# Kernel optimization log

Hardware: AMD Instinct MI355X
Metric: run time of the kernel (lower is better)

The kernel has to match this reference:

```python
import jax, jax.numpy as jnp
import numpy as np

B, N, D = 4, 2048, 1024
H, HD = 16, 64
MAX_SEQ = 4096
INNER = H * HD


def setup_inputs() -> dict:
    key = jax.random.key(0)
    ks = jax.random.split(key, 5)
    s = 0.02
    return {
        "x": jax.random.normal(ks[0], (B, N, D), dtype=jnp.float32),
        "ln_gamma": jnp.ones((D,), jnp.float32),
        "ln_beta": jnp.zeros((D,), jnp.float32),
        "w_qkv": jax.random.normal(ks[1], (D, 3 * INNER), dtype=jnp.float32) * s,
        "w_out": jax.random.normal(ks[2], (INNER, D), dtype=jnp.float32) * s,
        "b_out": jnp.zeros((D,), jnp.float32),
    }


def _rope_tables(n, head_dim):
    inv_freq = 1.0 / (10000.0 ** (jnp.arange(0, head_dim, 2, dtype=jnp.float32) / head_dim))
    pos = jnp.arange(n, dtype=jnp.float32)
    ang = pos[:, None] * inv_freq[None, :]  # [n, hd/2]
    return jnp.sin(ang), jnp.cos(ang)


def reference(x, ln_gamma, ln_beta, w_qkv, w_out, b_out):
    b, n, d = x.shape
    # LayerNorm
    mu = jnp.mean(x, axis=-1, keepdims=True)
    var = jnp.var(x, axis=-1, keepdims=True)
    xn = (x - mu) / jnp.sqrt(var + 1e-5) * ln_gamma + ln_beta
    # QKV projection (no bias)
    qkv = xn @ w_qkv  # [b, n, 3*inner]
    q, k, v = jnp.split(qkv, 3, axis=-1)
    def to_heads(t):
        return t.reshape(b, n, H, HD).transpose(0, 2, 1, 3)  # b h n d
    q, k, v = to_heads(q), to_heads(k), to_heads(v)
    # RoPE (half-split rotation, as in source)
    sin, cos = _rope_tables(n, HD)  # [n, hd/2]
    sin = sin[None, None]
    cos = cos[None, None]
    half = HD // 2
    def rotate(t):
        t1, t2 = t[..., :half], t[..., half:]
        return jnp.concatenate([t1 * cos - t2 * sin, t2 * cos + t1 * sin], axis=-1)
    qr, kr = rotate(q), rotate(k)
    scale = HD ** -0.5
    scores = jnp.einsum('bhid,bhjd->bhij', qr, kr) * scale
    probs = jax.nn.softmax(scores, axis=-1)
    out = jnp.einsum('bhij,bhjd->bhid', probs, v)
    out = out.transpose(0, 2, 1, 3).reshape(b, n, INNER)
    return out @ w_out + b_out
```

## Files before the change

kernel.cpp:

```cpp
#include <hip/hip_runtime.h>
#include <hip/hip_bf16.h>

#define Bb   4
#define Nn   2048
#define Dd   1024
#define Hh   16
#define HDd  64
#define IN3  3072
#define RR   8192

typedef __attribute__((ext_vector_type(8))) short short8;
typedef __attribute__((ext_vector_type(4))) short short4v;
typedef __attribute__((ext_vector_type(4))) float floatx4;

#define MFMA16(a, b, c) __builtin_amdgcn_mfma_f32_16x16x32_bf16((a), (b), (c), 0, 0, 0)

static __device__ __forceinline__ floatx4 mfma16x16x16(short4v a, short4v b, floatx4 c) {
#if __has_builtin(__builtin_amdgcn_mfma_f32_16x16x16bf16_1k)
    return __builtin_amdgcn_mfma_f32_16x16x16bf16_1k(a, b, c, 0, 0, 0);
#else
    floatx4 d;
    asm("v_mfma_f32_16x16x16_bf16 %0, %1, %2, %3" : "=v"(d) : "v"(a), "v"(b), "v"(c));
    return d;
#endif
}

static __device__ __forceinline__ unsigned short f2bf(float f) {
    union { float f; unsigned int u; } v; v.f = f;
    unsigned int r = v.u + 0x7fffu + ((v.u >> 16) & 1u);
    return (unsigned short)(r >> 16);
}
static __device__ __forceinline__ float bf2f(unsigned short h) {
    union { unsigned int u; float f; } v; v.u = ((unsigned int)h) << 16;
    return v.f;
}

static __device__ __forceinline__ float fast_exp2(float x) {
#if __has_builtin(__builtin_amdgcn_exp2f)
    return __builtin_amdgcn_exp2f(x);
#else
    return exp2f(x);
#endif
}

typedef const __attribute__((address_space(1))) void* gas1_t;
typedef __attribute__((address_space(3))) void* las3_t;
static __device__ __forceinline__ void load_lds16(const void* g, void* l) {
    __builtin_amdgcn_global_load_lds((gas1_t)(unsigned long long)g,
                                     (las3_t)(unsigned int)(unsigned long long)l,
                                     16, 0, 0);
}

__global__ void transpose_w(const float* __restrict__ src, unsigned short* __restrict__ dst,
                            int rows, int cols) {
    __shared__ float tile[32][33];
    int c0 = blockIdx.x * 32, r0 = blockIdx.y * 32;
    int tx = threadIdx.x, ty = threadIdx.y;
#pragma unroll
    for (int i = 0; i < 4; ++i) tile[ty + 8 * i][tx] = src[(r0 + ty + 8 * i) * cols + c0 + tx];
    __syncthreads();
#pragma unroll
    for (int i = 0; i < 4; ++i) dst[(c0 + ty + 8 * i) * rows + r0 + tx] = f2bf(tile[tx][ty + 8 * i]);
}

__global__ __launch_bounds__(256) void ln_kernel(const float* __restrict__ x,
                                                 const float* __restrict__ g,
                                                 const float* __restrict__ be,
                                                 unsigned short* __restrict__ xn) {
    int row = blockIdx.x, t = threadIdx.x;
    float4 v = ((const float4*)(x + row * Dd))[t];
    float s  = v.x + v.y + v.z + v.w;
    float sq = v.x * v.x + v.y * v.y + v.z * v.z + v.w * v.w;
#pragma unroll
    for (int off = 1; off < 64; off <<= 1) { s += __shfl_xor(s, off); sq += __shfl_xor(sq, off); }
    __shared__ float ps[4], pq2[4];
    int wv = t >> 6;
    if ((t & 63) == 0) { ps[wv] = s; pq2[wv] = sq; }
    __syncthreads();
    s  = ps[0] + ps[1] + ps[2] + ps[3];
    sq = pq2[0] + pq2[1] + pq2[2] + pq2[3];
    float mu   = s * (1.0f / Dd);
    float var  = sq * (1.0f / Dd) - mu * mu;
    float rstd = rsqrtf(var + 1e-5f);
    float4 gg = ((const float4*)g)[t];
    float4 bb = ((const float4*)be)[t];
    ushort4 o;
    o.x = f2bf((v.x - mu) * rstd * gg.x + bb.x);
    o.y = f2bf((v.y - mu) * rstd * gg.y + bb.y);
    o.z = f2bf((v.z - mu) * rstd * gg.z + bb.z);
    o.w = f2bf((v.w - mu) * rstd * gg.w + bb.w);
    ((ushort4*)(xn + row * Dd))[t] = o;
}

__global__ __launch_bounds__(256) void gemm_qkv(const unsigned short* __restrict__ A,
                                                const unsigned short* __restrict__ Bt,
                                                unsigned short* __restrict__ qo,
                                                unsigned short* __restrict__ ko,
                                                unsigned short* __restrict__ vo) {
    __shared__ unsigned short As[128 * 64];
    __shared__ unsigned short Bs[128 * 64];
    int r0 = blockIdx.x * 128, c0 = blockIdx.y * 128;
    int tid = threadIdx.x;
    int wave = tid >> 6, lane = tid & 63, l15 = lane & 15, quad = lane >> 4;
    int wm = wave & 1, wn = wave >> 1;
    floatx4 acc[4][4] = {};
    int srow8 = lane >> 3;
    int scol  = (lane & 7) * 8;
    for (int k0 = 0; k0 < 1024; k0 += 64) {
#pragma unroll
        for (int i = 0; i < 4; ++i) {
            int row = (wave * 4 + i) * 8 + srow8;
            load_lds16(&A[(r0 + row) * 1024 + k0 + scol],  &As[row * 64 + scol]);
            load_lds16(&Bt[(c0 + row) * 1024 + k0 + scol], &Bs[row * 64 + scol]);
        }
        __syncthreads();
#pragma unroll
        for (int ks = 0; ks < 2; ++ks) {
            short8 af[4], bf[4];
#pragma unroll
            for (int mi = 0; mi < 4; ++mi)
                af[mi] = *(const short8*)&As[(wm * 64 + mi * 16 + l15) * 64 + ks * 32 + quad * 8];
#pragma unroll
            for (int ni = 0; ni < 4; ++ni)
                bf[ni] = *(const short8*)&Bs[(wn * 64 + ni * 16 + l15) * 64 + ks * 32 + quad * 8];
#pragma unroll
            for (int mi = 0; mi < 4; ++mi)
#pragma unroll
                for (int ni = 0; ni < 4; ++ni)
                    acc[mi][ni] = MFMA16(af[mi], bf[ni], acc[mi][ni]);
        }
        __syncthreads();
    }
    unsigned short* outp = (c0 < 1024) ? qo : (c0 < 2048) ? ko : vo;
#pragma unroll
    for (int ni = 0; ni < 4; ++ni) {
        int c = c0 + wn * 64 + ni * 16 + l15;
        int cin = c & 1023;
        int h = cin >> 6, j = cin & 63;
#pragma unroll
        for (int mi = 0; mi < 4; ++mi) {
#pragma unroll
            for (int r2 = 0; r2 < 4; ++r2) {
                int rr = r0 + wm * 64 + mi * 16 + quad * 4 + r2;
                int b = rr >> 11, n = rr & 2047;
                int bh = b * 16 + h;
                outp[(bh * 2048 + n) * 64 + j] = f2bf(acc[mi][ni][r2]);
            }
        }
    }
}

__global__ __launch_bounds__(256) void vtrans(const unsigned short* __restrict__ v,
                                              unsigned short* __restrict__ vt) {
    __shared__ unsigned short T[64][72];
    int bh = blockIdx.y, n0 = blockIdx.x * 64;
    int t = threadIdx.x;
    int nl = t >> 2, c = (t & 3) * 16;
    const unsigned short* src = v + ((bh * 2048) + n0 + nl) * 64 + c;
    *(short8*)&T[nl][c]     = *(const short8*)src;
    *(short8*)&T[nl][c + 8] = *(const short8*)(src + 8);
    __syncthreads();
    int hd = t >> 2, nc = (t & 3) * 16;
    unsigned short tmp[16];
#pragma unroll
    for (int i = 0; i < 16; ++i) tmp[i] = T[nc + i][hd];
    unsigned short* dst = vt + ((bh * 64) + hd) * 2048 + n0 + nc;
    *(short8*)dst       = *(const short8*)&tmp[0];
    *(short8*)(dst + 8) = *(const short8*)&tmp[8];
}

__global__ __launch_bounds__(256) void rope_kernel(unsigned short* __restrict__ q,
                                                   unsigned short* __restrict__ k) {
    int idx = blockIdx.x * 256 + threadIdx.x;
    int j  = idx & 31;
    int n  = (idx >> 5) & 2047;
    int bh = idx >> 16;
    int base = (bh * 2048 + n) * 64;
    float inv = exp2f(-(float)j * (13.287712379549449f / 32.0f));
    float ang = (float)n * inv;
    float sa = sinf(ang), ca = cosf(ang);
    float q1 = bf2f(q[base + j]), q2 = bf2f(q[base + j + 32]);
    q[base + j]      = f2bf(q1 * ca - q2 * sa);
    q[base + j + 32] = f2bf(q2 * ca + q1 * sa);
    float k1 = bf2f(k[base + j]), k2 = bf2f(k[base + j + 32]);
    k[base + j]      = f2bf(k1 * ca - k2 * sa);
    k[base + j + 32] = f2bf(k2 * ca + k1 * sa);
}

__global__ __launch_bounds__(256, 4) void attn_kernel(const unsigned short* __restrict__ q,
                                                      const unsigned short* __restrict__ k,
                                                      const unsigned short* __restrict__ vt,
                                                      unsigned short* __restrict__ attn) {
    __shared__ unsigned short KVs[2][2][64 * 64];
    int bh = blockIdx.y, q0 = blockIdx.x * 128;
    int tid = threadIdx.x;
    int wave = tid >> 6, lane = tid & 63, l15 = lane & 15, quad = lane >> 4;
    const unsigned short* qb  = q  + bh * (Nn * HDd);
    const unsigned short* kbp = k  + bh * (Nn * HDd);
    const unsigned short* vb  = vt + bh * (HDd * Nn);
    int qbase = q0 + wave * 32;

    short8 bq[2][2];
#pragma unroll
    for (int g = 0; g < 2; ++g) {
        bq[g][0] = *(const short8*)&qb[(qbase + g * 16 + l15) * 64 + quad * 8];
        bq[g][1] = *(const short8*)&qb[(qbase + g * 16 + l15) * 64 + 32 + quad * 8];
    }

    auto stage = [&](int buf, int kb0) {
#pragma unroll
        for (int i = 0; i < 2; ++i) {
            int c = wave * 2 + i;
            int p = c * 64 + lane;
            int row = p >> 3, pr = p & 7;
            int sc = pr ^ (row & 7);
            load_lds16(&kbp[(kb0 + row) * 64 + sc * 8], &KVs[buf][0][p * 8]);
            load_lds16(&vb[row * Nn + kb0 + sc * 8],    &KVs[buf][1][p * 8]);
        }
    };

    floatx4 ot[2][4] = {};
    float l_run[2] = {0.0f, 0.0f};
    const float sc2 = 0.125f * 1.4426950408889634f;
    int swz0 = (quad ^ (l15 & 7)) << 3;
    int swz1 = ((4 | quad) ^ (l15 & 7)) << 3;
    int voff[4];
#pragma unroll
    for (int ks = 0; ks < 4; ++ks)
        voff[ks] = l15 * 64 + (((ks * 2) + (quad >> 1)) ^ (l15 & 7)) * 8 + (quad & 1) * 4;

    auto body = [&](int cur, int kt) {
        if (kt < 31) stage(cur ^ 1, (kt + 1) * 64);
        const unsigned short* Kc = KVs[cur][0];
        const unsigned short* Vc = KVs[cur][1];
        short8 ka0[4], ka1[4];
#pragma unroll
        for (int mb = 0; mb < 4; ++mb) {
            ka0[mb] = *(const short8*)&Kc[(mb * 16 + l15) * 64 + swz0];
            ka1[mb] = *(const short8*)&Kc[(mb * 16 + l15) * 64 + swz1];
        }
        floatx4 st[2][4];
#pragma unroll
        for (int g = 0; g < 2; ++g)
#pragma unroll
            for (int mb = 0; mb < 4; ++mb) {
                floatx4 z = {0.0f, 0.0f, 0.0f, 0.0f};
                z = MFMA16(ka0[mb], bq[g][0], z);
                st[g][mb] = MFMA16(ka1[mb], bq[g][1], z);
            }
        short4v pa[2][4];
#pragma unroll
        for (int g = 0; g < 2; ++g) {
            float sump = 0.0f;
#pragma unroll
            for (int mb = 0; mb < 4; ++mb) {
                float p0 = fast_exp2(st[g][mb][0] * sc2);
                float p1 = fast_exp2(st[g][mb][1] * sc2);
                float p2 = fast_exp2(st[g][mb][2] * sc2);
                float p3 = fast_exp2(st[g][mb][3] * sc2);
                sump += (p0 + p1) + (p2 + p3);
                union { ushort4 u; short4v s; } w;
                *(__hip_bfloat162*)&w.u.x = __float22bfloat162_rn(float2{p0, p1});
                *(__hip_bfloat162*)&w.u.z = __float22bfloat162_rn(float2{p2, p3});
                pa[g][mb] = w.s;
            }
            l_run[g] += sump;
        }
#pragma unroll
        for (int ht = 0; ht < 4; ++ht)
#pragma unroll
            for (int ks = 0; ks < 4; ++ks) {
                short4v bv = *(const short4v*)&Vc[ht * 1024 + voff[ks]];
#pragma unroll
                for (int g = 0; g < 2; ++g)
                    ot[g][ht] = mfma16x16x16(pa[g][ks], bv, ot[g][ht]);
            }
        __syncthreads();
    };

    stage(0, 0);
    __syncthreads();
    for (int kt = 0; kt < 32; kt += 2) {
        body(0, kt);
        body(1, kt + 1);
    }
    float il[2][4];
#pragma unroll
    for (int g = 0; g < 2; ++g) {
        float l = l_run[g];
        l += __shfl_xor(l, 16);
        l += __shfl_xor(l, 32);
        float invl = 1.0f / l;
#pragma unroll
        for (int r = 0; r < 4; ++r) il[g][r] = __shfl(invl, quad * 4 + r);
    }
    unsigned short* ob = ((unsigned short*)KVs) + wave * 4096;
#pragma unroll
    for (int g = 0; g < 2; ++g)
#pragma unroll
        for (int ht = 0; ht < 4; ++ht)
#pragma unroll
            for (int r = 0; r < 4; ++r)
                ob[(g * 16 + quad * 4 + r) * 72 + ht * 16 + l15] = f2bf(ot[g][ht][r] * il[g][r]);
    int b = bh >> 4, h = bh & 15;
#pragma unroll
    for (int pass = 0; pass < 2; ++pass) {
        int q_loc = pass * 16 + (lane >> 2), seg = lane & 3;
        unsigned short* dst = attn + ((long)(b * Nn + q0 + wave * 32 + q_loc)) * 1024 + h * 64 + seg * 16;
        *(short8*)dst       = *(const short8*)&ob[q_loc * 72 + seg * 16];
        *(short8*)(dst + 8) = *(const short8*)&ob[q_loc * 72 + seg * 16 + 8];
    }
}

__global__ __launch_bounds__(256) void gemm_out(const unsigned short* __restrict__ A,
                                                const unsigned short* __restrict__ Bt,
                                                const float* __restrict__ bout,
                                                float* __restrict__ out) {
    __shared__ unsigned short As[128 * 64];
    __shared__ unsigned short Bs[128 * 64];
    int r0 = blockIdx.x * 128, c0 = blockIdx.y * 128;
    int tid = threadIdx.x;
    int wave = tid >> 6, lane = tid & 63, l15 = lane & 15, quad = lane >> 4;
    int wm = wave & 1, wn = wave >> 1;
    floatx4 acc[4][4] = {};
    int srow8 = lane >> 3;
    int scol  = (lane & 7) * 8;
    for (int k0 = 0; k0 < 1024; k0 += 64) {
#pragma unroll
        for (int i = 0; i < 4; ++i) {
            int row = (wave * 4 + i) * 8 + srow8;
            load_lds16(&A[(r0 + row) * 1024 + k0 + scol],  &As[row * 64 + scol]);
            load_lds16(&Bt[(c0 + row) * 1024 + k0 + scol], &Bs[row * 64 + scol]);
        }
        __syncthreads();
#pragma unroll
        for (int ks = 0; ks < 2; ++ks) {
            short8 af[4], bf[4];
#pragma unroll
            for (int mi = 0; mi < 4; ++mi)
                af[mi] = *(const short8*)&As[(wm * 64 + mi * 16 + l15) * 64 + ks * 32 + quad * 8];
#pragma unroll
            for (int ni = 0; ni < 4; ++ni)
                bf[ni] = *(const short8*)&Bs[(wn * 64 + ni * 16 + l15) * 64 + ks * 32 + quad * 8];
#pragma unroll
            for (int mi = 0; mi < 4; ++mi)
#pragma unroll
                for (int ni = 0; ni < 4; ++ni)
                    acc[mi][ni] = MFMA16(af[mi], bf[ni], acc[mi][ni]);
        }
        __syncthreads();
    }
#pragma unroll
    for (int ni = 0; ni < 4; ++ni) {
        int c = c0 + wn * 64 + ni * 16 + l15;
        float bias = bout[c];
#pragma unroll
        for (int mi = 0; mi < 4; ++mi)
#pragma unroll
            for (int r2 = 0; r2 < 4; ++r2) {
                int rr = r0 + wm * 64 + mi * 16 + quad * 4 + r2;
                out[rr * 1024 + c] = acc[mi][ni][r2] + bias;
            }
    }
}

extern "C" void kernel_launch(void* const* d_in, const int* in_sizes, int n_in,
                              void* d_out, int out_size, void* d_ws, size_t ws_size,
                              hipStream_t stream) {
    const float* x    = (const float*)d_in[0];
    const float* g    = (const float*)d_in[1];
    const float* be   = (const float*)d_in[2];
    const float* wqkv = (const float*)d_in[3];
    const float* wout = (const float*)d_in[4];
    const float* bout = (const float*)d_in[5];
    float* out = (float*)d_out;

    char* ws = (char*)d_ws;
    unsigned short* xn    = (unsigned short*)(ws);
    unsigned short* wqkvT = (unsigned short*)(ws + 16777216);
    unsigned short* woutT = (unsigned short*)(ws + 23068672);
    unsigned short* qb    = (unsigned short*)(ws + 25165824);
    unsigned short* kb    = (unsigned short*)(ws + 41943040);
    unsigned short* vt    = (unsigned short*)(ws + 58720256);
    unsigned short* attn  = (unsigned short*)(ws + 75497472);
    unsigned short* vtmp  = attn;

    transpose_w<<<dim3(IN3 / 32, Dd / 32), dim3(32, 8), 0, stream>>>(wqkv, wqkvT, Dd, IN3);
    transpose_w<<<dim3(Dd / 32, Dd / 32), dim3(32, 8), 0, stream>>>(wout, woutT, Dd, Dd);
    ln_kernel<<<RR, 256, 0, stream>>>(x, g, be, xn);
    gemm_qkv<<<dim3(RR / 128, IN3 / 128), 256, 0, stream>>>(xn, wqkvT, qb, kb, vtmp);
    vtrans<<<dim3(Nn / 64, Bb * Hh), 256, 0, stream>>>(vtmp, vt);
    rope_kernel<<<(64 * 2048 * 32) / 256, 256, 0, stream>>>(qb, kb);
    attn_kernel<<<dim3(Nn / 128, Bb * Hh), 256, 0, stream>>>(qb, kb, vt, attn);
    gemm_out<<<dim3(RR / 128, Dd / 128), 256, 0, stream>>>(attn, woutT, bout, out);
}
```

Baseline: 313.3 us.

## Use 16x16x32 MFMA for PV by permuting V transpose layout

Replaces the PV product's 16x16x16 bf16 MFMAs with 16x16x32 MFMAs fed by 8-element P and V fragments. To make the P register layout match the K-dimension ordering, the V transpose kernel permutes key positions within each 32-chunk. This halves the PV MFMA instruction count and turns the V LDS reads into wider 16-byte loads. It also raises the attention kernel's minimum-blocks hint from 4 to 5, which may force register spills.

```diff
diff --git a/kernel.cpp b/kernel.cpp
--- a/kernel.cpp
+++ b/kernel.cpp
@@ -10,20 +10,9 @@
 #define RR   8192
 
 typedef __attribute__((ext_vector_type(8))) short short8;
-typedef __attribute__((ext_vector_type(4))) short short4v;
 typedef __attribute__((ext_vector_type(4))) float floatx4;
 
 #define MFMA16(a, b, c) __builtin_amdgcn_mfma_f32_16x16x32_bf16((a), (b), (c), 0, 0, 0)
-
-static __device__ __forceinline__ floatx4 mfma16x16x16(short4v a, short4v b, floatx4 c) {
-#if __has_builtin(__builtin_amdgcn_mfma_f32_16x16x16bf16_1k)
-    return __builtin_amdgcn_mfma_f32_16x16x16bf16_1k(a, b, c, 0, 0, 0);
-#else
-    floatx4 d;
-    asm("v_mfma_f32_16x16x16_bf16 %0, %1, %2, %3" : "=v"(d) : "v"(a), "v"(b), "v"(c));
-    return d;
-#endif
-}
 
 static __device__ __forceinline__ unsigned short f2bf(float f) {
     union { float f; unsigned int u; } v; v.f = f;
@@ -163,7 +152,12 @@
     int hd = t >> 2, nc = (t & 3) * 16;
     unsigned short tmp[16];
 #pragma unroll
-    for (int i = 0; i < 16; ++i) tmp[i] = T[nc + i][hd];
+    for (int i = 0; i < 16; ++i) {
+        int pos = nc + i;
+        int blk = pos >> 5, p = pos & 31;
+        int kq = (p >> 3) & 3, hh = (p >> 2) & 1, r = p & 3;
+        tmp[i] = T[blk * 32 + hh * 16 + kq * 4 + r][hd];
+    }
     unsigned short* dst = vt + ((bh * 64) + hd) * 2048 + n0 + nc;
     *(short8*)dst       = *(const short8*)&tmp[0];
     *(short8*)(dst + 8) = *(const short8*)&tmp[8];
@@ -187,7 +181,7 @@
     k[base + j + 32] = f2bf(k2 * ca + k1 * sa);
 }
 
-__global__ __launch_bounds__(256, 4) void attn_kernel(const unsigned short* __restrict__ q,
+__global__ __launch_bounds__(256, 5) void attn_kernel(const unsigned short* __restrict__ q,
                                                       const unsigned short* __restrict__ k,
                                                       const unsigned short* __restrict__ vt,
                                                       unsigned short* __restrict__ attn) {
@@ -224,10 +218,6 @@
     const float sc2 = 0.125f * 1.4426950408889634f;
     int swz0 = (quad ^ (l15 & 7)) << 3;
     int swz1 = ((4 | quad) ^ (l15 & 7)) << 3;
-    int voff[4];
-#pragma unroll
-    for (int ks = 0; ks < 4; ++ks)
-        voff[ks] = l15 * 64 + (((ks * 2) + (quad >> 1)) ^ (l15 & 7)) * 8 + (quad & 1) * 4;
 
     auto body = [&](int cur, int kt) {
         if (kt < 31) stage(cur ^ 1, (kt + 1) * 64);
@@ -248,33 +238,39 @@
                 z = MFMA16(ka0[mb], bq[g][0], z);
                 st[g][mb] = MFMA16(ka1[mb], bq[g][1], z);
             }
-        short4v pa[2][4];
+        short8 pa[2][2];
 #pragma unroll
         for (int g = 0; g < 2; ++g) {
             float sump = 0.0f;
 #pragma unroll
-            for (int mb = 0; mb < 4; ++mb) {
-                float p0 = fast_exp2(st[g][mb][0] * sc2);
-                float p1 = fast_exp2(st[g][mb][1] * sc2);
-                float p2 = fast_exp2(st[g][mb][2] * sc2);
-                float p3 = fast_exp2(st[g][mb][3] * sc2);
-                sump += (p0 + p1) + (p2 + p3);
-                union { ushort4 u; short4v s; } w;
-                *(__hip_bfloat162*)&w.u.x = __float22bfloat162_rn(float2{p0, p1});
-                *(__hip_bfloat162*)&w.u.z = __float22bfloat162_rn(float2{p2, p3});
-                pa[g][mb] = w.s;
+            for (int c = 0; c < 2; ++c) {
+                union { ushort4 u[2]; short8 s; } w;
+#pragma unroll
+                for (int t2 = 0; t2 < 2; ++t2) {
+                    int mb = 2 * c + t2;
+                    float p0 = fast_exp2(st[g][mb][0] * sc2);
+                    float p1 = fast_exp2(st[g][mb][1] * sc2);
+                    float p2 = fast_exp2(st[g][mb][2] * sc2);
+                    float p3 = fast_exp2(st[g][mb][3] * sc2);
+                    sump += (p0 + p1) + (p2 + p3);
+                    *(__hip_bfloat162*)&w.u[t2].x = __float22bfloat162_rn(float2{p0, p1});
+                    *(__hip_bfloat162*)&w.u[t2].z = __float22bfloat162_rn(float2{p2, p3});
+                }
+                pa[g][c] = w.s;
             }
             l_run[g] += sump;
         }
 #pragma unroll
-        for (int ht = 0; ht < 4; ++ht)
-#pragma unroll
-            for (int ks = 0; ks < 4; ++ks) {
-                short4v bv = *(const short4v*)&Vc[ht * 1024 + voff[ks]];
-#pragma unroll
-                for (int g = 0; g < 2; ++g)
-                    ot[g][ht] = mfma16x16x16(pa[g][ks], bv, ot[g][ht]);
-            }
+        for (int ht = 0; ht < 4; ++ht) {
+            int row = (ht * 16 + l15) * 64;
+            short8 bv0 = *(const short8*)&Vc[row + swz0];
+            short8 bv1 = *(const short8*)&Vc[row + swz1];
+#pragma unroll
+            for (int g = 0; g < 2; ++g) {
+                ot[g][ht] = MFMA16(pa[g][0], bv0, ot[g][ht]);
+                ot[g][ht] = MFMA16(pa[g][1], bv1, ot[g][ht]);
+            }
+        }
         __syncthreads();
     };
 
```

Measured after the change: 469.5 us. 49.9% more time.
